# Performance work log

Measured on AMD Instinct MI355X. Metric: run time of the kernel, lower is better.

Reference implementation:

```python
import jax, jax.numpy as jnp
import numpy as np

N_BASE = 4          # len('NACGT'[1:])
STATE_LEN = 5
S = N_BASE ** STATE_LEN   # 1024 states
NZ = N_BASE + 1           # 5 transitions per state
T_STEPS = 800
BATCH = 32


def _build_idx():
    # idx[i] = [i, 0*256 + i//4, 1*256 + i//4, 2*256 + i//4, 3*256 + i//4]
    i = np.arange(S)
    trans = np.stack([j * (S // N_BASE) + i // N_BASE for j in range(N_BASE)], axis=1)
    idx = np.concatenate([i[:, None], trans], axis=1).astype(np.int64)      # (S, NZ)
    # transposed transition structure (stable sort: duplicates grouped deterministically)
    idx_T = np.argsort(idx.ravel(), kind='stable').reshape(S, NZ)
    idx_T_div = idx_T // NZ
    return jnp.asarray(idx), jnp.asarray(idx_T), jnp.asarray(idx_T_div)


def _scan(Ms, idx, v0):
    """Log-semiring recurrence: alpha[t+1] = logsumexp(Ms[t] + alpha[t][:, idx], -1).
    Ms: (T, N, S, NZ); idx: (S, NZ); v0: (N, S). Returns (T+1, N, S)."""
    def step(alpha, M):
        nxt = jax.scipy.special.logsumexp(M + alpha[:, idx], axis=-1)  # (N, S)
        return nxt, nxt
    _, alphas = jax.lax.scan(step, v0, Ms)
    return jnp.concatenate([v0[None], alphas], axis=0)


def setup_inputs() -> dict:
    key = jax.random.key(0)
    scores = jax.random.normal(key, (T_STEPS, BATCH, S * NZ), dtype=jnp.float32)
    return {"scores": scores}


def reference(scores):
    idx, idx_T, idx_T_div = _build_idx()
    T, N, _ = scores.shape
    Ms = scores.reshape(T, N, S, NZ)
    v0 = jnp.zeros((N, S), scores.dtype)   # semiring Log.one == 0.0
    # forward scores
    fwd = _scan(Ms, idx, v0)                                   # (T+1, N, S)
    # backward scores: gather transposed transitions, run scan in reverse time
    Ms_T = scores[:, :, idx_T]                                 # (T, N, S, NZ)
    bwd = jnp.flip(_scan(jnp.flip(Ms_T, 0), idx_T_div, v0), 0)  # (T+1, N, S)
    posts = jax.nn.softmax(fwd + bwd, axis=-1)                 # (T+1, N, S)
    return (jnp.swapaxes(scores, 0, 1),
            jnp.swapaxes(bwd, 0, 1),
            jnp.swapaxes(posts, 0, 1))
```

## Files before the change

### kernel.cpp

```cpp
#include <hip/hip_runtime.h>

#define T_STEPS 800
#define NBATCH  32
#define SST     1024
#define ROW     5120
#define DEPTH   8

#define SCAN_BLOCKS 64
#define COPY_BLOCKS 1536
#define GRID (SCAN_BLOCKS + COPY_BLOCKS)

__device__ __forceinline__ float lse5(float v0, float v1, float v2, float v3, float v4) {
  float m = fmaxf(fmaxf(fmaxf(v0, v1), fmaxf(v2, v3)), v4);
  float s = __expf(v0 - m) + __expf(v1 - m) + __expf(v2 - m) +
            __expf(v3 - m) + __expf(v4 - m);
  return m + __logf(s);
}

__device__ __forceinline__ void sync_lds() {
  asm volatile("s_waitcnt lgkmcnt(0)" ::: "memory");
  __builtin_amdgcn_s_barrier();
  asm volatile("" ::: "memory");
}

template <int DIR>
__device__ __forceinline__ void prefetch(const float* __restrict__ base, int step, int u,
                                         float* __restrict__ r, float* __restrict__ s) {
  const int t = DIR ? (T_STEPS - 1 - step) : step;
  const float* rp = base + (size_t)t * (NBATCH * ROW);
#pragma unroll
  for (int m = 0; m < 5; ++m)
    *(float4*)&r[4 * m] = *(const float4*)&rp[20 * u + 4 * m];
  if (DIR) {
#pragma unroll
    for (int j = 0; j < 4; ++j) s[j] = rp[5 * u + 1280 * j];
  }
}

template <int DIR>
__device__ void scan_run(const float* __restrict__ scores, float* __restrict__ out,
                         int n, float (*abuf)[SST]) {
  const int u = threadIdx.x;
  const float* base = scores + (size_t)n * ROW;
  float* outn = out + (size_t)n * (T_STEPS + 1) * SST;

  float a[4] = {0.f, 0.f, 0.f, 0.f};

  float v[DEPTH][20];
  float s5[DEPTH][4];
#pragma unroll
  for (int i = 0; i < DEPTH; ++i) prefetch<DIR>(base, i, u, v[i], s5[i]);

  abuf[0][u] = 0.f; abuf[0][u + 256] = 0.f; abuf[0][u + 512] = 0.f; abuf[0][u + 768] = 0.f;
  {
    const float4 z = {0.f, 0.f, 0.f, 0.f};
    const size_t t0 = DIR ? (size_t)T_STEPS : 0;
    ((float4*)(outn + t0 * SST))[u] = z;
  }
  sync_lds();

  for (int p = 0; p < T_STEPS; p += DEPTH) {
#pragma unroll
    for (int i = 0; i < DEPTH; ++i) {
      const int step = p + i;
      const int cur = step & 1;
      const int nxt = cur ^ 1;

      float4 pv;
      if (DIR == 0) {
        pv.x = abuf[cur][u];
        pv.y = abuf[cur][u + 256];
        pv.z = abuf[cur][u + 512];
        pv.w = abuf[cur][u + 768];
      } else {
        pv = *(const float4*)&abuf[cur][4 * u];
      }

      float na[4];
#pragma unroll
      for (int j = 0; j < 4; ++j) {
        float v0, v1, v2, v3, v4;
        if (DIR == 0) {
          v0 = v[i][5 * j + 0] + a[j];
          v1 = v[i][5 * j + 1] + pv.x;
          v2 = v[i][5 * j + 2] + pv.y;
          v3 = v[i][5 * j + 3] + pv.z;
          v4 = v[i][5 * j + 4] + pv.w;
        } else {
          v0 = s5[i][j]          + a[j];
          v1 = v[i][1 + j + 0]   + pv.x;
          v2 = v[i][1 + j + 5]   + pv.y;
          v3 = v[i][1 + j + 10]  + pv.z;
          v4 = v[i][1 + j + 15]  + pv.w;
        }
        na[j] = lse5(v0, v1, v2, v3, v4);
      }

      if (step + DEPTH < T_STEPS) prefetch<DIR>(base, step + DEPTH, u, v[i], s5[i]);

      if (DIR == 0) {
        const float4 o = {na[0], na[1], na[2], na[3]};
        ((float4*)(outn + (size_t)(step + 1) * SST))[u] = o;
        *(float4*)&abuf[nxt][4 * u] = o;
      } else {
        const int t = T_STEPS - 1 - step;
#pragma unroll
        for (int j = 0; j < 4; ++j) {
          outn[(size_t)t * SST + u + 256 * j] = na[j];
          abuf[nxt][u + 256 * j] = na[j];
        }
      }
#pragma unroll
      for (int j = 0; j < 4; ++j) a[j] = na[j];

      sync_lds();
    }
  }
}

__global__ __launch_bounds__(256, 1) void mega(const float* __restrict__ scores,
                                               float* __restrict__ out0,
                                               float* __restrict__ bwdo,
                                               float* __restrict__ fposts) {
  __shared__ float abuf[2][SST];
  const int b = blockIdx.x;
  if (b < SCAN_BLOCKS) {
    if (b < NBATCH) scan_run<0>(scores, fposts, b, abuf);
    else            scan_run<1>(scores, bwdo,   b - NBATCH, abuf);
  } else {
    const int tb = b - SCAN_BLOCKS;
    for (int r = tb; r < NBATCH * T_STEPS; r += COPY_BLOCKS) {
      const int t = r / NBATCH, n = r % NBATCH;
      const float4* src = (const float4*)(scores + (size_t)r * ROW);
      float4* dst = (float4*)(out0 + ((size_t)n * T_STEPS + t) * ROW);
#pragma unroll
      for (int i = 0; i < 5; ++i)
        dst[threadIdx.x + 256 * i] = src[threadIdx.x + 256 * i];
    }
  }
}

__global__ __launch_bounds__(256) void posts_kernel(float* __restrict__ fp,
                                                    const float* __restrict__ bp) {
  const int lane = threadIdx.x & 63;
  const int wid  = threadIdx.x >> 6;
  const size_t row = (size_t)blockIdx.x * 4 + wid;
  float* f = fp + row * SST;
  const float* b = bp + row * SST;

  float x[16];
#pragma unroll
  for (int k = 0; k < 4; ++k) {
    const float4 fv = ((const float4*)f)[lane + 64 * k];
    const float4 bv = ((const float4*)b)[lane + 64 * k];
    x[4 * k + 0] = fv.x + bv.x;
    x[4 * k + 1] = fv.y + bv.y;
    x[4 * k + 2] = fv.z + bv.z;
    x[4 * k + 3] = fv.w + bv.w;
  }
  float m = x[0];
#pragma unroll
  for (int j = 1; j < 16; ++j) m = fmaxf(m, x[j]);
#pragma unroll
  for (int off = 32; off >= 1; off >>= 1) m = fmaxf(m, __shfl_xor(m, off));
  float ssum = 0.0f;
#pragma unroll
  for (int j = 0; j < 16; ++j) { x[j] = __expf(x[j] - m); ssum += x[j]; }
#pragma unroll
  for (int off = 32; off >= 1; off >>= 1) ssum += __shfl_xor(ssum, off);
  const float inv = 1.0f / ssum;
#pragma unroll
  for (int k = 0; k < 4; ++k) {
    float4 o;
    o.x = x[4 * k + 0] * inv;
    o.y = x[4 * k + 1] * inv;
    o.z = x[4 * k + 2] * inv;
    o.w = x[4 * k + 3] * inv;
    ((float4*)f)[lane + 64 * k] = o;
  }
}

extern "C" void kernel_launch(void* const* d_in, const int* in_sizes, int n_in,
                              void* d_out, int out_size, void* d_ws, size_t ws_size,
                              hipStream_t stream) {
  (void)in_sizes; (void)n_in; (void)d_ws; (void)ws_size; (void)out_size;
  const float* scores = (const float*)d_in[0];
  float* out = (float*)d_out;
  float* out0   = out;
  float* bwdo   = out + (size_t)NBATCH * T_STEPS * ROW;
  float* fposts = bwdo + (size_t)NBATCH * (T_STEPS + 1) * SST;

  mega<<<GRID, 256, 0, stream>>>(scores, out0, bwdo, fposts);
  posts_kernel<<<(NBATCH * (T_STEPS + 1)) / 4, 256, 0, stream>>>(fposts, bwdo);
}
```

Before: 820.7 us.

## Fuse scores transpose copy into forward scan, drop copy blocks, pin prefetch scheduling

Removes the 1536 separate copy blocks and has the forward scan blocks write the swapped-axes scores output from the rows they already hold in registers. Prefetch depth drops from 8 to 5, and the loads are issued after the step's stores, fenced by sched_barrier so the compiler cannot reorder them. This avoids a second full read of scores and keeps the copy blocks from competing with the latency-bound scans for bandwidth. In exchange the 32 forward blocks now carry all the output write traffic, and the shallower prefetch may expose more load latency.

```diff
diff --git a/kernel.cpp b/kernel.cpp
--- a/kernel.cpp
+++ b/kernel.cpp
@@ -4,11 +4,9 @@
 #define NBATCH  32
 #define SST     1024
 #define ROW     5120
-#define DEPTH   8
+#define DEPTH   5
 
-#define SCAN_BLOCKS 64
-#define COPY_BLOCKS 1536
-#define GRID (SCAN_BLOCKS + COPY_BLOCKS)
+#define PIN() __builtin_amdgcn_sched_barrier(0)
 
 __device__ __forceinline__ float lse5(float v0, float v1, float v2, float v3, float v4) {
   float m = fmaxf(fmaxf(fmaxf(v0, v1), fmaxf(v2, v3)), v4);
@@ -17,57 +15,67 @@
   return m + __logf(s);
 }
 
-__device__ __forceinline__ void sync_lds() {
+__device__ __forceinline__ void barrier_lgkm() {
   asm volatile("s_waitcnt lgkmcnt(0)" ::: "memory");
   __builtin_amdgcn_s_barrier();
   asm volatile("" ::: "memory");
 }
 
 template <int DIR>
-__device__ __forceinline__ void prefetch(const float* __restrict__ base, int step, int u,
-                                         float* __restrict__ r, float* __restrict__ s) {
-  const int t = DIR ? (T_STEPS - 1 - step) : step;
+__device__ __forceinline__ void issue(const float* __restrict__ base, int s, int u,
+                                      float4 (&vi)[5], float (&si)[4]) {
+  const int t = DIR ? (T_STEPS - 1 - s) : s;
   const float* rp = base + (size_t)t * (NBATCH * ROW);
+  const float4* r4 = (const float4*)(rp + 20 * u);
 #pragma unroll
-  for (int m = 0; m < 5; ++m)
-    *(float4*)&r[4 * m] = *(const float4*)&rp[20 * u + 4 * m];
-  if (DIR) {
+  for (int m = 0; m < 5; ++m) vi[m] = r4[m];
+  if constexpr (DIR) {
 #pragma unroll
-    for (int j = 0; j < 4; ++j) s[j] = rp[5 * u + 1280 * j];
+    for (int j = 0; j < 4; ++j) si[j] = rp[5 * u + 1280 * j];
   }
 }
 
 template <int DIR>
 __device__ void scan_run(const float* __restrict__ scores, float* __restrict__ out,
-                         int n, float (*abuf)[SST]) {
+                         float* __restrict__ out0, int n, float (*abuf)[SST]) {
   const int u = threadIdx.x;
   const float* base = scores + (size_t)n * ROW;
   float* outn = out + (size_t)n * (T_STEPS + 1) * SST;
+  float* o0n  = out0 + (size_t)n * T_STEPS * ROW;
 
-  float a[4] = {0.f, 0.f, 0.f, 0.f};
+  float4 v[DEPTH][5];
+  float  s5[DEPTH][4];
+  float  a[4] = {0.f, 0.f, 0.f, 0.f};
 
-  float v[DEPTH][20];
-  float s5[DEPTH][4];
+  PIN();
 #pragma unroll
-  for (int i = 0; i < DEPTH; ++i) prefetch<DIR>(base, i, u, v[i], s5[i]);
+  for (int i = 0; i < DEPTH; ++i) issue<DIR>(base, i, u, v[i], s5[i]);
+  PIN();
 
-  abuf[0][u] = 0.f; abuf[0][u + 256] = 0.f; abuf[0][u + 512] = 0.f; abuf[0][u + 768] = 0.f;
   {
     const float4 z = {0.f, 0.f, 0.f, 0.f};
+    *(float4*)&abuf[0][4 * u] = z;
     const size_t t0 = DIR ? (size_t)T_STEPS : 0;
     ((float4*)(outn + t0 * SST))[u] = z;
   }
-  sync_lds();
+  barrier_lgkm();
 
   for (int p = 0; p < T_STEPS; p += DEPTH) {
 #pragma unroll
     for (int i = 0; i < DEPTH; ++i) {
-      const int step = p + i;
-      const int cur = step & 1;
+      const int s = p + i;
+      const int cur = s & 1;
       const int nxt = cur ^ 1;
 
+      float fv[20];
+#pragma unroll
+      for (int m = 0; m < 5; ++m) {
+        fv[4 * m + 0] = v[i][m].x; fv[4 * m + 1] = v[i][m].y;
+        fv[4 * m + 2] = v[i][m].z; fv[4 * m + 3] = v[i][m].w;
+      }
+
       float4 pv;
-      if (DIR == 0) {
+      if constexpr (!DIR) {
         pv.x = abuf[cur][u];
         pv.y = abuf[cur][u + 256];
         pv.z = abuf[cur][u + 512];
@@ -79,41 +87,47 @@
       float na[4];
 #pragma unroll
       for (int j = 0; j < 4; ++j) {
-        float v0, v1, v2, v3, v4;
-        if (DIR == 0) {
-          v0 = v[i][5 * j + 0] + a[j];
-          v1 = v[i][5 * j + 1] + pv.x;
-          v2 = v[i][5 * j + 2] + pv.y;
-          v3 = v[i][5 * j + 3] + pv.z;
-          v4 = v[i][5 * j + 4] + pv.w;
+        float w0, w1, w2, w3, w4;
+        if constexpr (!DIR) {
+          w0 = fv[5 * j + 0] + a[j];
+          w1 = fv[5 * j + 1] + pv.x;
+          w2 = fv[5 * j + 2] + pv.y;
+          w3 = fv[5 * j + 3] + pv.z;
+          w4 = fv[5 * j + 4] + pv.w;
         } else {
-          v0 = s5[i][j]          + a[j];
-          v1 = v[i][1 + j + 0]   + pv.x;
-          v2 = v[i][1 + j + 5]   + pv.y;
-          v3 = v[i][1 + j + 10]  + pv.z;
-          v4 = v[i][1 + j + 15]  + pv.w;
+          w0 = s5[i][j]       + a[j];
+          w1 = fv[1 + j + 0]  + pv.x;
+          w2 = fv[1 + j + 5]  + pv.y;
+          w3 = fv[1 + j + 10] + pv.z;
+          w4 = fv[1 + j + 15] + pv.w;
         }
-        na[j] = lse5(v0, v1, v2, v3, v4);
+        na[j] = lse5(w0, w1, w2, w3, w4);
+        a[j] = na[j];
       }
 
-      if (step + DEPTH < T_STEPS) prefetch<DIR>(base, step + DEPTH, u, v[i], s5[i]);
-
-      if (DIR == 0) {
+      if constexpr (!DIR) {
         const float4 o = {na[0], na[1], na[2], na[3]};
-        ((float4*)(outn + (size_t)(step + 1) * SST))[u] = o;
+        ((float4*)(outn + (size_t)(s + 1) * SST))[u] = o;
         *(float4*)&abuf[nxt][4 * u] = o;
+        float4* o0 = (float4*)(o0n + (size_t)s * ROW + 20 * u);
+#pragma unroll
+        for (int m = 0; m < 5; ++m) o0[m] = v[i][m];
       } else {
-        const int t = T_STEPS - 1 - step;
+        const int t = T_STEPS - 1 - s;
 #pragma unroll
         for (int j = 0; j < 4; ++j) {
           outn[(size_t)t * SST + u + 256 * j] = na[j];
           abuf[nxt][u + 256 * j] = na[j];
         }
       }
-#pragma unroll
-      for (int j = 0; j < 4; ++j) a[j] = na[j];
 
-      sync_lds();
+      if (s + DEPTH < T_STEPS) {
+        PIN();
+        issue<DIR>(base, s + DEPTH, u, v[i], s5[i]);
+        PIN();
+      }
+
+      barrier_lgkm();
     }
   }
 }
@@ -124,20 +138,8 @@
                                                float* __restrict__ fposts) {
   __shared__ float abuf[2][SST];
   const int b = blockIdx.x;
-  if (b < SCAN_BLOCKS) {
-    if (b < NBATCH) scan_run<0>(scores, fposts, b, abuf);
-    else            scan_run<1>(scores, bwdo,   b - NBATCH, abuf);
-  } else {
-    const int tb = b - SCAN_BLOCKS;
-    for (int r = tb; r < NBATCH * T_STEPS; r += COPY_BLOCKS) {
-      const int t = r / NBATCH, n = r % NBATCH;
-      const float4* src = (const float4*)(scores + (size_t)r * ROW);
-      float4* dst = (float4*)(out0 + ((size_t)n * T_STEPS + t) * ROW);
-#pragma unroll
-      for (int i = 0; i < 5; ++i)
-        dst[threadIdx.x + 256 * i] = src[threadIdx.x + 256 * i];
-    }
-  }
+  if (b < NBATCH) scan_run<0>(scores, fposts, out0, b, abuf);
+  else            scan_run<1>(scores, bwdo,   out0, b - NBATCH, abuf);
 }
 
 __global__ __launch_bounds__(256) void posts_kernel(float* __restrict__ fp,
@@ -190,6 +192,6 @@
   float* bwdo   = out + (size_t)NBATCH * T_STEPS * ROW;
   float* fposts = bwdo + (size_t)NBATCH * (T_STEPS + 1) * SST;
 
-  mega<<<GRID, 256, 0, stream>>>(scores, out0, bwdo, fposts);
+  mega<<<2 * NBATCH, 256, 0, stream>>>(scores, out0, bwdo, fposts);
   posts_kernel<<<(NBATCH * (T_STEPS + 1)) / 4, 256, 0, stream>>>(fposts, bwdo);
 }
```

Result: slower. 1.105 ms (+34.6%).
